# Performance work log

Hardware: AMD Instinct MI355X
Metric: run time of the kernel (lower is better)

The kernel has to match this reference:

```python
import jax, jax.numpy as jnp
import numpy as np

D_MODEL = 2048
NUM_HEADS = 16
HEAD_DIM = D_MODEL // NUM_HEADS
B, S = 2, 2048


def rotate_half(x):
    x1, x2 = jnp.split(x, 2, axis=-1)
    return jnp.concatenate((-x2, x1), axis=-1)


def setup_inputs() -> dict:
    key = jax.random.key(0)
    ks = jax.random.split(key, 7)
    x = jax.random.normal(ks[0], (B, S, D_MODEL), dtype=jnp.float32)
    cos = jax.random.normal(ks[1], (1, 1, S, HEAD_DIM), dtype=jnp.float32)
    sin = jax.random.normal(ks[2], (1, 1, S, HEAD_DIM), dtype=jnp.float32)
    scale = 1.0 / np.sqrt(D_MODEL)
    Wq = jax.random.normal(ks[3], (D_MODEL, D_MODEL), dtype=jnp.float32) * scale
    Wk = jax.random.normal(ks[4], (D_MODEL, D_MODEL), dtype=jnp.float32) * scale
    Wv = jax.random.normal(ks[5], (D_MODEL, D_MODEL), dtype=jnp.float32) * scale
    Wo = jax.random.normal(ks[6], (D_MODEL, D_MODEL), dtype=jnp.float32) * scale
    return {"x": x, "cos": cos, "sin": sin, "Wq": Wq, "Wk": Wk, "Wv": Wv, "Wo": Wo}


def reference(x, cos, sin, Wq, Wk, Wv, Wo):
    Bb, Ss, Dd = x.shape
    H, hd = NUM_HEADS, HEAD_DIM
    # nn.Linear: y = x @ W.T ; here W stored as [out, in]
    q = (x @ Wq.T).reshape(Bb, Ss, H, hd).transpose(0, 2, 1, 3)  # [B,H,S,hd]
    k = (x @ Wk.T).reshape(Bb, Ss, H, hd).transpose(0, 2, 1, 3)
    v = (x @ Wv.T).reshape(Bb, Ss, H, hd).transpose(0, 2, 1, 3)
    q = q * cos + rotate_half(q) * sin
    k = k * cos + rotate_half(k) * sin
    scale = 1.0 / jnp.sqrt(jnp.asarray(hd, dtype=x.dtype))
    scores = jnp.einsum('bhqd,bhkd->bhqk', q, k) * scale  # [B,H,S,S]
    causal = jnp.tril(jnp.ones((Ss, Ss), dtype=bool))
    scores = jnp.where(causal[None, None], scores, jnp.finfo(x.dtype).min)
    attn = jax.nn.softmax(scores, axis=-1)
    out = jnp.einsum('bhqk,bhkd->bhqd', attn, v)  # [B,H,S,hd]
    out = out.transpose(0, 2, 1, 3).reshape(Bb, Ss, Dd)
    return out @ Wo.T
```

## Files before the change

### kernel.cpp

```cpp
#include <hip/hip_runtime.h>

typedef unsigned short u16;
typedef __attribute__((ext_vector_type(8))) short bf8v;
typedef __attribute__((ext_vector_type(4))) float f4v;

#define DEV static __device__ __forceinline__

DEV float bf2f(u16 u){ unsigned x = ((unsigned)u) << 16; float f; __builtin_memcpy(&f, &x, 4); return f; }
DEV u16 f2bf(float f){ unsigned x; __builtin_memcpy(&x, &f, 4); x += 0x7fff + ((x >> 16) & 1); return (u16)(x >> 16); }

DEV void async16(const void* g, void* l){
  __builtin_amdgcn_global_load_lds((const __attribute__((address_space(1))) unsigned*)g,
                                   (__attribute__((address_space(3))) unsigned*)l, 16, 0, 0);
}

DEV void vwait8(){ asm volatile("s_waitcnt vmcnt(8)" ::: "memory"); }
DEV void vwait6(){ asm volatile("s_waitcnt vmcnt(6)" ::: "memory"); }
DEV void vwait0(){ asm volatile("s_waitcnt vmcnt(0)" ::: "memory"); }
DEV void bar(){ asm volatile("s_barrier" ::: "memory"); }

__global__ __launch_bounds__(256) void f2b_k(const float* __restrict__ src,
                                             u16* __restrict__ dst)
{
  const long i = ((long)blockIdx.x * 256 + threadIdx.x) * 4;
  const float4 v = *(const float4*)(src + i);
  ushort4 o;
  o.x = f2bf(v.x); o.y = f2bf(v.y); o.z = f2bf(v.z); o.w = f2bf(v.w);
  *(ushort4*)(dst + i) = o;
}

__global__ __launch_bounds__(256) void f2b3_k(const float* __restrict__ a,
                                              const float* __restrict__ b,
                                              const float* __restrict__ c,
                                              u16* __restrict__ dst)
{
  const int bx = blockIdx.x;
  const float* s = bx < 4096 ? a : (bx < 8192 ? b : c);
  const long soff = ((long)(bx & 4095) * 256 + threadIdx.x) * 4;
  const long doff = ((long)bx * 256 + threadIdx.x) * 4;
  const float4 v = *(const float4*)(s + soff);
  ushort4 o;
  o.x = f2bf(v.x); o.y = f2bf(v.y); o.z = f2bf(v.z); o.w = f2bf(v.w);
  *(ushort4*)(dst + doff) = o;
}

constexpr int KDIM = 2048;

__global__ __launch_bounds__(512, 2) void gemm256(const u16* __restrict__ A,
                                                  const u16* __restrict__ B,
                                                  u16* __restrict__ C0,
                                                  u16* __restrict__ C1,
                                                  u16* __restrict__ C2,
                                                  float* __restrict__ Cf, int mode)
{
  __shared__ __align__(16) u16 Asm[3][8192];
  __shared__ __align__(16) u16 Bsm[3][16384];

  const int tid = threadIdx.x;
  const int w = tid >> 6, lane = tid & 63;
  const int ln = lane & 15, quad = lane >> 4;
  const int wr = w >> 2, wc = w & 3;

  const int gx = gridDim.x;
  const int nwg = gx * gridDim.y;
  const int wg = blockIdx.y * gx + blockIdx.x;
  const int swz = (wg & 7) * (nwg >> 3) + (wg >> 3);
  const int bx = swz % gx, by = swz / gx;
  const long m0 = (long)by << 7, n0 = (long)bx << 8;

  f4v acc[4][4] = {};

  const u16* pA  = A + (m0 + w * 16 + ln) * (long)KDIM + quad * 8;
  const u16* pB0 = B + (n0 + w * 16 + ln) * (long)KDIM + quad * 8;
  const u16* pB1 = B + (n0 + (8 + w) * 16 + ln) * (long)KDIM + quad * 8;
  char* ldsA = (char*)Asm + (long)tid * 16;
  char* ldsB = (char*)Bsm + (long)tid * 16;

#define STG(sl, ks, kt) do{                                                     \
    async16(pA  + (kt) + (ks) * 32, ldsA + (sl) * 16384 + (ks) * 8192);         \
    async16(pB0 + (kt) + (ks) * 32, ldsB + (sl) * 32768 + (ks) * 16384);        \
    async16(pB1 + (kt) + (ks) * 32, ldsB + (sl) * 32768 + (ks) * 16384 + 8192); \
  }while(0)

  STG(0, 0, 0);  STG(0, 1, 0);
  STG(1, 0, 64); STG(1, 1, 64);
  vwait6();
  bar();

  int s0 = 0, s1 = 1, s2 = 2;
  const int nt = KDIM / 64;
  for (int t = 0; t < nt; ++t) {
    const u16* Ab = Asm[s0];
    const u16* Bb = Bsm[s0];
    const bool st = (t + 2 < nt);
    const long kt2 = (long)(t + 2) * 64;

    bf8v a0[4], b0[4];
#pragma unroll
    for (int i = 0; i < 4; ++i) a0[i] = *(const bf8v*)&Ab[((wr * 4 + i) * 64 + lane) * 8];
#pragma unroll
    for (int j = 0; j < 4; ++j) b0[j] = *(const bf8v*)&Bb[((wc * 4 + j) * 64 + lane) * 8];
    if (st) STG(s2, 0, kt2);
    bar();
    __builtin_amdgcn_s_setprio(1);
#pragma unroll
    for (int i = 0; i < 4; ++i)
#pragma unroll
      for (int j = 0; j < 4; ++j)
        acc[i][j] = __builtin_amdgcn_mfma_f32_16x16x32_bf16(a0[i], b0[j], acc[i][j], 0, 0, 0);
    __builtin_amdgcn_s_setprio(0);
    bar();

    bf8v a1[4], b1[4];
#pragma unroll
    for (int i = 0; i < 4; ++i) a1[i] = *(const bf8v*)&Ab[((8 + wr * 4 + i) * 64 + lane) * 8];
#pragma unroll
    for (int j = 0; j < 4; ++j) b1[j] = *(const bf8v*)&Bb[((16 + wc * 4 + j) * 64 + lane) * 8];
    if (st) STG(s2, 1, kt2);
    if (st) vwait6(); else vwait0();
    bar();
    __builtin_amdgcn_s_setprio(1);
#pragma unroll
    for (int i = 0; i < 4; ++i)
#pragma unroll
      for (int j = 0; j < 4; ++j)
        acc[i][j] = __builtin_amdgcn_mfma_f32_16x16x32_bf16(a1[i], b1[j], acc[i][j], 0, 0, 0);
    __builtin_amdgcn_s_setprio(0);
    bar();

    const int tmp = s0; s0 = s1; s1 = s2; s2 = tmp;
  }
#undef STG

#pragma unroll
  for (int i = 0; i < 4; i++) {
    const long mrow = m0 + wr * 64 + i * 16 + quad * 4;
#pragma unroll
    for (int j = 0; j < 4; j++) {
      const long ncol = n0 + wc * 64 + j * 16 + ln;
#pragma unroll
      for (int r = 0; r < 4; r++) {
        const float fv = acc[i][j][r];
        const long m = mrow + r;
        if (mode == 0) {
          C0[m * 2048 + ncol] = f2bf(fv);
        } else if (mode == 2) {
          Cf[m * 2048 + ncol] = fv;
        } else if (mode == 1) {
          const long s = m & 2047, bb = m >> 11;
          const long hh = ncol >> 7, dc = ncol & 127;
          C0[((bb * 16 + hh) * 128 + dc) * 2048 + s] = f2bf(fv);
        } else {
          const int sec = (int)(n0 >> 11);
          const long nc = ncol & 2047;
          if (sec == 0)      C0[m * 2048 + nc] = f2bf(fv);
          else if (sec == 1) C1[m * 2048 + nc] = f2bf(fv);
          else {
            const long s = m & 2047, bb = m >> 11;
            const long hh = nc >> 7, dc = nc & 127;
            C2[((bb * 16 + hh) * 128 + dc) * 2048 + s] = f2bf(fv);
          }
        }
      }
    }
  }
}

__global__ __launch_bounds__(256) void rope2_k(u16* __restrict__ qb,
                                               u16* __restrict__ kb,
                                               const float* __restrict__ cs,
                                               const float* __restrict__ sn)
{
  const long idx = (long)blockIdx.x * 256 + threadIdx.x;
  u16* t = (idx >= 4194304) ? kb : qb;
  const long i2 = idx & 4194303;
  const long m = i2 >> 10;
  const int rest = (int)(i2 & 1023);
  const int h = rest >> 6, d = rest & 63;
  const int s = (int)(m & 2047);
  const long base = m * 2048 + h * 128 + d;
  const float a  = bf2f(t[base]), b = bf2f(t[base + 64]);
  const float c1 = cs[s * 128 + d],      s1 = sn[s * 128 + d];
  const float c2 = cs[s * 128 + d + 64], s2 = sn[s * 128 + d + 64];
  t[base]      = f2bf(a * c1 - b * s1);
  t[base + 64] = f2bf(b * c2 + a * s2);
}

__global__ __launch_bounds__(512) void attn_k(const u16* __restrict__ q,
                                              const u16* __restrict__ k,
                                              const u16* __restrict__ vt,
                                              u16* __restrict__ ao)
{
  __shared__ __align__(16) u16 Ks[2][16384];
  __shared__ __align__(16) u16 Vs[2][16384];
  __shared__ __align__(16) u16 Ps[8 * 16 * 72];
  const int xa = blockIdx.x;
  const int bh = blockIdx.y;
  const int b = bh >> 4, h = bh & 15;
  const int tid = threadIdx.x;
  const int w = tid >> 6, lane = tid & 63;
  const int ln = lane & 15, quad = lane >> 4;

  const u16* kb0 = k + ((long)(b * 2048 + (tid & 15))) * 2048 + h * 128
                     + ((tid >> 6) & 3) * 32 + ((tid >> 4) & 3) * 8;
  const u16* vb0 = vt + ((long)(bh * 128 + (tid & 15))) * 2048
                      + ((tid >> 6) & 1) * 32 + ((tid >> 4) & 3) * 8;
  const int tb = (tid >> 7) & 1;
  const int bit8 = tid >> 8;
  int krow[4]; long voff[4];
#pragma unroll
  for (int it2 = 0; it2 < 4; ++it2) {
    const int ie = 2 * it2 + bit8;
    krow[it2] = (ie >> 2) * 64 + (ie & 3) * 16;
    const int g = 2 * ie + tb;
    voff[it2] = (long)((g & 7) * 16) * 2048 + (g >> 3) * 64;
  }

#define STK(sl, k0) do{                                                          \
    _Pragma("unroll")                                                            \
    for (int it2 = 0; it2 < 4; ++it2)                                            \
      async16(kb0 + (long)((k0) + krow[it2]) * 2048,                             \
              (char*)&Ks[sl][0] + it2 * 8192 + w * 1024);                        \
  }while(0)
#define STV(sl, k0) do{                                                          \
    _Pragma("unroll")                                                            \
    for (int it2 = 0; it2 < 4; ++it2)                                            \
      async16(vb0 + voff[it2] + (k0),                                            \
              (char*)&Vs[sl][0] + it2 * 8192 + w * 1024);                        \
  }while(0)

  const short one_bf = (short)0x3F80;
  const bf8v vones = {one_bf, one_bf, one_bf, one_bf, one_bf, one_bf, one_bf, one_bf};
  const float scl = 0.08838834764831845f;
  const float shift = 20.0f;
  const int wbase = w * 16 * 72;
  const int qts[2] = {15 - xa, xa};

  for (int tix = 0; tix < 2; ++tix) {
    const int qt = qts[tix];
    const int q0 = qt << 7;

    bf8v aq[4];
    {
      const u16* qp = q + ((long)(b * 2048 + q0 + w * 16 + ln)) * 2048 + h * 128;
#pragma unroll
      for (int dt = 0; dt < 4; ++dt) aq[dt] = *(const bf8v*)(qp + dt * 32 + quad * 8);
    }
    f4v O[8] = {};
    f4v Osum = {};

    STK(0, 0); STV(0, 0);

    for (int ktp = 0; ktp <= qt; ++ktp) {
      const int k0s = ktp << 7;
      const bool lastit = (ktp == qt);
      const int sl = ktp & 1;
      if (!lastit) { STK(sl ^ 1, k0s + 128); STV(sl ^ 1, k0s + 128); }
      if (!lastit) vwait8(); else vwait0();
      bar();
      const u16* Kb = &Ks[sl][0];
      const u16* Vb = &Vs[sl][0];

      f4v S[8];
#pragma unroll
      for (int jt = 0; jt < 8; jt++) {
        const int jb = (jt >> 2) * 64 + (jt & 3) * 16;
        if (lastit && jb > w * 16 + 15) {
          S[jt] = (f4v){-1e30f, -1e30f, -1e30f, -1e30f};
          continue;
        }
        const int sub = jt >> 2, jl = jt & 3;
        f4v s = {};
#pragma unroll
        for (int dt = 0; dt < 4; dt++) {
          const bf8v bk = *(const bf8v*)&Kb[(sub * 1024 + (jl * 4 + dt) * 64 + lane) * 8];
          s = __builtin_amdgcn_mfma_f32_16x16x32_bf16(aq[dt], bk, s, 0, 0, 0);
        }
        S[jt] = s;
      }
      if (lastit) {
        const int qi = w * 16 + quad * 4;
#pragma unroll
        for (int jt = 0; jt < 8; jt++) {
          const int dcol = (jt >> 2) * 64 + (jt & 3) * 16 + ln;
#pragma unroll
          for (int r = 0; r < 4; r++) {
            const float arg = (dcol > qi + r) ? -1e30f : (S[jt][r] * scl - shift);
            S[jt][r] = __expf(arg);
          }
        }
      } else {
#pragma unroll
        for (int jt = 0; jt < 8; jt++)
#pragma unroll
          for (int r = 0; r < 4; r++) S[jt][r] = __expf(S[jt][r] * scl - shift);
      }

#pragma unroll
      for (int sub = 0; sub < 2; ++sub) {
        if (sub == 1 && lastit && w < 4) break;
#pragma unroll
        for (int jl = 0; jl < 4; jl++)
#pragma unroll
          for (int r = 0; r < 4; r++)
            Ps[wbase + (quad * 4 + r) * 72 + jl * 16 + ln] = f2bf(S[sub * 4 + jl][r]);
        bf8v ap[2];
#pragma unroll
        for (int k2 = 0; k2 < 2; k2++)
          ap[k2] = *(const bf8v*)&Ps[wbase + ln * 72 + k2 * 32 + quad * 8];
#pragma unroll
        for (int nt = 0; nt < 8; nt++) {
#pragma unroll
          for (int k2 = 0; k2 < 2; k2++) {
            const bf8v bv = *(const bf8v*)&Vb[(sub * 1024 + (nt * 2 + k2) * 64 + lane) * 8];
            O[nt] = __builtin_amdgcn_mfma_f32_16x16x32_bf16(ap[k2], bv, O[nt], 0, 0, 0);
          }
        }
#pragma unroll
        for (int k2 = 0; k2 < 2; k2++)
          Osum = __builtin_amdgcn_mfma_f32_16x16x32_bf16(ap[k2], vones, Osum, 0, 0, 0);
      }
      bar();
    }

    float inv[4];
#pragma unroll
    for (int r = 0; r < 4; r++) inv[r] = 1.0f / Osum[r];
    const long ob = ((long)(b * 2048 + q0 + w * 16 + quad * 4)) * 2048 + h * 128 + ln;
#pragma unroll
    for (int r = 0; r < 4; r++)
#pragma unroll
      for (int nt = 0; nt < 8; nt++)
        ao[ob + (long)r * 2048 + nt * 16] = f2bf(O[nt][r] * inv[r]);
  }
#undef STK
#undef STV
}

extern "C" void kernel_launch(void* const* d_in, const int* in_sizes, int n_in,
                              void* d_out, int out_size, void* d_ws, size_t ws_size,
                              hipStream_t stream) {
  const float* x  = (const float*)d_in[0];
  const float* cs = (const float*)d_in[1];
  const float* sn = (const float*)d_in[2];
  const float* Wq = (const float*)d_in[3];
  const float* Wk = (const float*)d_in[4];
  const float* Wv = (const float*)d_in[5];
  const float* Wo = (const float*)d_in[6];
  float* out = (float*)d_out;

  const size_t E = 4194304;
  u16* xb = (u16*)d_ws;

  const size_t need = 11 * E * sizeof(u16);
  if (ws_size >= need) {
    u16* wqkv = xb + 2 * E;
    u16* qb   = wqkv + 3 * E;
    u16* kb   = qb + 2 * E;
    u16* vtb  = kb + 2 * E;
    u16* aob  = xb;

    f2b_k<<<8192, 256, 0, stream>>>(x, xb);
    f2b3_k<<<12288, 256, 0, stream>>>(Wq, Wk, Wv, wqkv);
    gemm256<<<dim3(24, 32), 512, 0, stream>>>(xb, wqkv, qb, kb, vtb, nullptr, 3);
    rope2_k<<<32768, 256, 0, stream>>>(qb, kb, cs, sn);
    attn_k<<<dim3(8, 32), 512, 0, stream>>>(qb, kb, vtb, aob);
    f2b_k<<<4096, 256, 0, stream>>>(Wo, wqkv);
    gemm256<<<dim3(8, 32), 512, 0, stream>>>(aob, wqkv, nullptr, nullptr, nullptr, out, 2);
  } else {
    u16* wb  = xb + 2 * E;
    u16* qb  = wb + E;
    u16* kb  = qb + 2 * E;
    u16* vtb = kb + 2 * E;
    u16* aob = xb;

    f2b_k<<<8192, 256, 0, stream>>>(x, xb);
    f2b_k<<<4096, 256, 0, stream>>>(Wq, wb);
    gemm256<<<dim3(8, 32), 512, 0, stream>>>(xb, wb, qb, nullptr, nullptr, nullptr, 0);
    f2b_k<<<4096, 256, 0, stream>>>(Wk, wb);
    gemm256<<<dim3(8, 32), 512, 0, stream>>>(xb, wb, kb, nullptr, nullptr, nullptr, 0);
    f2b_k<<<4096, 256, 0, stream>>>(Wv, wb);
    gemm256<<<dim3(8, 32), 512, 0, stream>>>(xb, wb, vtb, nullptr, nullptr, nullptr, 1);
    rope2_k<<<32768, 256, 0, stream>>>(qb, kb, cs, sn);
    attn_k<<<dim3(8, 32), 512, 0, stream>>>(qb, kb, vtb, aob);
    f2b_k<<<4096, 256, 0, stream>>>(Wo, wb);
    gemm256<<<dim3(8, 32), 512, 0, stream>>>(aob, wb, nullptr, nullptr, nullptr, out, 2);
  }
}
```

Before: 478.9 us.

## Add 256x256-tile GEMM with split-phase pipelining for Q/K projection

Adds a new GEMM kernel that computes 256x256 output tiles with a double-buffered LDS pipeline, staging quarter-tiles of A and B interleaved with four MFMA phases. The fused QKV projection is split so that the Q and K columns use this larger-tile kernel and the V columns, with their transposed store, keep the old 128x256 kernel via a new column offset argument. The intent is higher arithmetic intensity and less global/LDS traffic per FLOP for most of the projection. The cost is two launches instead of one, more accumulator registers, and a more intricate wait-count schedule that could stall or add risk.

```diff
diff --git a/kernel.cpp b/kernel.cpp
--- a/kernel.cpp
+++ b/kernel.cpp
@@ -17,6 +17,14 @@
 DEV void vwait8(){ asm volatile("s_waitcnt vmcnt(8)" ::: "memory"); }
 DEV void vwait6(){ asm volatile("s_waitcnt vmcnt(6)" ::: "memory"); }
 DEV void vwait0(){ asm volatile("s_waitcnt vmcnt(0)" ::: "memory"); }
+DEV void vw(int n){
+  switch(n){
+    case 8: asm volatile("s_waitcnt vmcnt(8)" ::: "memory"); break;
+    case 4: asm volatile("s_waitcnt vmcnt(4)" ::: "memory"); break;
+    case 2: asm volatile("s_waitcnt vmcnt(2)" ::: "memory"); break;
+    default: asm volatile("s_waitcnt vmcnt(0)" ::: "memory"); break;
+  }
+}
 DEV void bar(){ asm volatile("s_barrier" ::: "memory"); }
 
 __global__ __launch_bounds__(256) void f2b_k(const float* __restrict__ src,
@@ -46,15 +54,15 @@
 
 constexpr int KDIM = 2048;
 
-__global__ __launch_bounds__(512, 2) void gemm256(const u16* __restrict__ A,
-                                                  const u16* __restrict__ B,
-                                                  u16* __restrict__ C0,
-                                                  u16* __restrict__ C1,
-                                                  u16* __restrict__ C2,
-                                                  float* __restrict__ Cf, int mode)
+__global__ __launch_bounds__(512, 2) void gemmq(const u16* __restrict__ A,
+                                                const u16* __restrict__ B,
+                                                u16* __restrict__ C0,
+                                                u16* __restrict__ C1,
+                                                u16* __restrict__ C2,
+                                                float* __restrict__ Cf, int mode)
 {
-  __shared__ __align__(16) u16 Asm[3][8192];
-  __shared__ __align__(16) u16 Bsm[3][16384];
+  __shared__ __align__(16) u16 Asm[2][16384];
+  __shared__ __align__(16) u16 Bsm[2][16384];
 
   const int tid = threadIdx.x;
   const int w = tid >> 6, lane = tid & 63;
@@ -66,75 +74,128 @@
   const int wg = blockIdx.y * gx + blockIdx.x;
   const int swz = (wg & 7) * (nwg >> 3) + (wg >> 3);
   const int bx = swz % gx, by = swz / gx;
-  const long m0 = (long)by << 7, n0 = (long)bx << 8;
-
-  f4v acc[4][4] = {};
-
-  const u16* pA  = A + (m0 + w * 16 + ln) * (long)KDIM + quad * 8;
-  const u16* pB0 = B + (n0 + w * 16 + ln) * (long)KDIM + quad * 8;
-  const u16* pB1 = B + (n0 + (8 + w) * 16 + ln) * (long)KDIM + quad * 8;
-  char* ldsA = (char*)Asm + (long)tid * 16;
-  char* ldsB = (char*)Bsm + (long)tid * 16;
-
-#define STG(sl, ks, kt) do{                                                     \
-    async16(pA  + (kt) + (ks) * 32, ldsA + (sl) * 16384 + (ks) * 8192);         \
-    async16(pB0 + (kt) + (ks) * 32, ldsB + (sl) * 32768 + (ks) * 16384);        \
-    async16(pB1 + (kt) + (ks) * 32, ldsB + (sl) * 32768 + (ks) * 16384 + 8192); \
-  }while(0)
-
-  STG(0, 0, 0);  STG(0, 1, 0);
-  STG(1, 0, 64); STG(1, 1, 64);
-  vwait6();
+  const long m0 = (long)by << 8, n0 = (long)bx << 8;
+
+  f4v acc[8][4] = {};
+
+  const int q = w >> 1;
+  const int colb = (w & 1) * 32 + quad * 8;
+  long gArow[4], gBrow[4];
+  {
+    const int Ab4[4] = {0, 8, 4, 12};
+    const int Bb4[4] = {0, 8, 2, 10};
+#pragma unroll
+    for (int r = 0; r < 4; ++r) {
+      gArow[r] = (long)((Ab4[r] + q) * 16 + ln) * KDIM;
+      gBrow[r] = (long)((Bb4[r] + (q & 1) + (q >> 1) * 4) * 16 + ln) * KDIM;
+    }
+  }
+  const u16* gA = A + m0 * KDIM + colb;
+  const u16* gB = B + n0 * KDIM + colb;
+
+#define STAGE_A(sl, r, kt) async16(gA + gArow[r] + (kt), (char*)Asm + (sl)*32768 + (r)*8192 + w*1024)
+#define STAGE_B(sl, r, kt) async16(gB + gBrow[r] + (kt), (char*)Bsm + (sl)*32768 + (r)*8192 + w*1024)
+
+  STAGE_A(0,0,0);  STAGE_A(0,1,0);
+  STAGE_B(0,0,0);  STAGE_B(0,1,0);
+  STAGE_B(0,2,0);  STAGE_B(0,3,0);
+  STAGE_A(0,2,0);  STAGE_A(0,3,0);
+  STAGE_A(1,0,64); STAGE_A(1,1,64);
+  STAGE_B(1,0,64); STAGE_B(1,1,64);
+  vwait8();
   bar();
 
-  int s0 = 0, s1 = 1, s2 = 2;
   const int nt = KDIM / 64;
   for (int t = 0; t < nt; ++t) {
-    const u16* Ab = Asm[s0];
-    const u16* Bb = Bsm[s0];
-    const bool st = (t + 2 < nt);
-    const long kt2 = (long)(t + 2) * 64;
-
-    bf8v a0[4], b0[4];
-#pragma unroll
-    for (int i = 0; i < 4; ++i) a0[i] = *(const bf8v*)&Ab[((wr * 4 + i) * 64 + lane) * 8];
-#pragma unroll
-    for (int j = 0; j < 4; ++j) b0[j] = *(const bf8v*)&Bb[((wc * 4 + j) * 64 + lane) * 8];
-    if (st) STG(s2, 0, kt2);
-    bar();
+    const int cs = t & 1;
+    const u16* Ab = Asm[cs];
+    const u16* Bb = Bsm[cs];
+    int w1 = 8, w2 = 8, w3 = 8, w4 = 8;
+    if (t == nt - 2) { w4 = 4; }
+    else if (t == nt - 1) { w1 = 2; w2 = 0; w3 = 0; w4 = 0; }
+    const long kn1 = (long)(t + 1) * 64;
+    const long kn2 = (long)(t + 2) * 64;
+
+    bf8v aL[4][2], aH[4][2], bL[2][2], bH[2][2];
+
+#pragma unroll
+    for (int i = 0; i < 4; ++i) {
+      const int ib = (i + wr * 4) * 2;
+      aL[i][0] = *(const bf8v*)&Ab[((ib + 0) * 64 + lane) * 8];
+      aL[i][1] = *(const bf8v*)&Ab[((ib + 1) * 64 + lane) * 8];
+    }
+#pragma unroll
+    for (int j = 0; j < 2; ++j) {
+      const int jb = (j + wc * 2) * 2;
+      bL[j][0] = *(const bf8v*)&Bb[((jb + 0) * 64 + lane) * 8];
+      bL[j][1] = *(const bf8v*)&Bb[((jb + 1) * 64 + lane) * 8];
+    }
+    if (t + 1 < nt) { STAGE_B(cs ^ 1, 2, kn1); STAGE_B(cs ^ 1, 3, kn1); }
+    vw(w1); bar();
     __builtin_amdgcn_s_setprio(1);
 #pragma unroll
     for (int i = 0; i < 4; ++i)
 #pragma unroll
-      for (int j = 0; j < 4; ++j)
-        acc[i][j] = __builtin_amdgcn_mfma_f32_16x16x32_bf16(a0[i], b0[j], acc[i][j], 0, 0, 0);
+      for (int j = 0; j < 2; ++j) {
+        acc[i][j] = __builtin_amdgcn_mfma_f32_16x16x32_bf16(aL[i][0], bL[j][0], acc[i][j], 0, 0, 0);
+        acc[i][j] = __builtin_amdgcn_mfma_f32_16x16x32_bf16(aL[i][1], bL[j][1], acc[i][j], 0, 0, 0);
+      }
     __builtin_amdgcn_s_setprio(0);
-    bar();
-
-    bf8v a1[4], b1[4];
-#pragma unroll
-    for (int i = 0; i < 4; ++i) a1[i] = *(const bf8v*)&Ab[((8 + wr * 4 + i) * 64 + lane) * 8];
-#pragma unroll
-    for (int j = 0; j < 4; ++j) b1[j] = *(const bf8v*)&Bb[((16 + wc * 4 + j) * 64 + lane) * 8];
-    if (st) STG(s2, 1, kt2);
-    if (st) vwait6(); else vwait0();
-    bar();
+
+#pragma unroll
+    for (int j = 0; j < 2; ++j) {
+      const int jb = ((j & 1) + 8 + wc * 2) * 2;
+      bH[j][0] = *(const bf8v*)&Bb[((jb + 0) * 64 + lane) * 8];
+      bH[j][1] = *(const bf8v*)&Bb[((jb + 1) * 64 + lane) * 8];
+    }
+    if (t + 1 < nt) { STAGE_A(cs ^ 1, 2, kn1); STAGE_A(cs ^ 1, 3, kn1); }
+    vw(w2); bar();
     __builtin_amdgcn_s_setprio(1);
 #pragma unroll
     for (int i = 0; i < 4; ++i)
 #pragma unroll
-      for (int j = 0; j < 4; ++j)
-        acc[i][j] = __builtin_amdgcn_mfma_f32_16x16x32_bf16(a1[i], b1[j], acc[i][j], 0, 0, 0);
+      for (int j = 0; j < 2; ++j) {
+        acc[i][2 + j] = __builtin_amdgcn_mfma_f32_16x16x32_bf16(aL[i][0], bH[j][0], acc[i][2 + j], 0, 0, 0);
+        acc[i][2 + j] = __builtin_amdgcn_mfma_f32_16x16x32_bf16(aL[i][1], bH[j][1], acc[i][2 + j], 0, 0, 0);
+      }
     __builtin_amdgcn_s_setprio(0);
-    bar();
-
-    const int tmp = s0; s0 = s1; s1 = s2; s2 = tmp;
-  }
-#undef STG
-
-#pragma unroll
-  for (int i = 0; i < 4; i++) {
-    const long mrow = m0 + wr * 64 + i * 16 + quad * 4;
+
+#pragma unroll
+    for (int i = 0; i < 4; ++i) {
+      const int ib = (i + 8 + wr * 4) * 2;
+      aH[i][0] = *(const bf8v*)&Ab[((ib + 0) * 64 + lane) * 8];
+      aH[i][1] = *(const bf8v*)&Ab[((ib + 1) * 64 + lane) * 8];
+    }
+    if (t + 2 < nt) { STAGE_A(cs, 0, kn2); STAGE_A(cs, 1, kn2); }
+    vw(w3); bar();
+    __builtin_amdgcn_s_setprio(1);
+#pragma unroll
+    for (int i = 0; i < 4; ++i)
+#pragma unroll
+      for (int j = 0; j < 2; ++j) {
+        acc[4 + i][j] = __builtin_amdgcn_mfma_f32_16x16x32_bf16(aH[i][0], bL[j][0], acc[4 + i][j], 0, 0, 0);
+        acc[4 + i][j] = __builtin_amdgcn_mfma_f32_16x16x32_bf16(aH[i][1], bL[j][1], acc[4 + i][j], 0, 0, 0);
+      }
+    __builtin_amdgcn_s_setprio(0);
+
+    if (t + 2 < nt) { STAGE_B(cs, 0, kn2); STAGE_B(cs, 1, kn2); }
+    vw(w4); bar();
+    __builtin_amdgcn_s_setprio(1);
+#pragma unroll
+    for (int i = 0; i < 4; ++i)
+#pragma unroll
+      for (int j = 0; j < 2; ++j) {
+        acc[4 + i][2 + j] = __builtin_amdgcn_mfma_f32_16x16x32_bf16(aH[i][0], bH[j][0], acc[4 + i][2 + j], 0, 0, 0);
+        acc[4 + i][2 + j] = __builtin_amdgcn_mfma_f32_16x16x32_bf16(aH[i][1], bH[j][1], acc[4 + i][2 + j], 0, 0, 0);
+      }
+    __builtin_amdgcn_s_setprio(0);
+  }
+#undef STAGE_A
+#undef STAGE_B
+
+#pragma unroll
+  for (int i = 0; i < 8; i++) {
+    const long mrow = m0 + wr * 128 + i * 16 + quad * 4;
 #pragma unroll
     for (int j = 0; j < 4; j++) {
       const long ncol = n0 + wc * 64 + j * 16 + ln;
@@ -166,6 +227,127 @@
   }
 }
 
+__global__ __launch_bounds__(512, 2) void gemm256(const u16* __restrict__ A,
+                                                  const u16* __restrict__ B,
+                                                  u16* __restrict__ C0,
+                                                  u16* __restrict__ C1,
+                                                  u16* __restrict__ C2,
+                                                  float* __restrict__ Cf, int mode,
+                                                  int nofs)
+{
+  __shared__ __align__(16) u16 Asm[3][8192];
+  __shared__ __align__(16) u16 Bsm[3][16384];
+
+  const int tid = threadIdx.x;
+  const int w = tid >> 6, lane = tid & 63;
+  const int ln = lane & 15, quad = lane >> 4;
+  const int wr = w >> 2, wc = w & 3;
+
+  const int gx = gridDim.x;
+  const int nwg = gx * gridDim.y;
+  const int wg = blockIdx.y * gx + blockIdx.x;
+  const int swz = (wg & 7) * (nwg >> 3) + (wg >> 3);
+  const int bx = swz % gx, by = swz / gx;
+  const long m0 = (long)by << 7, n0 = ((long)bx << 8) + nofs;
+
+  f4v acc[4][4] = {};
+
+  const u16* pA  = A + (m0 + w * 16 + ln) * (long)KDIM + quad * 8;
+  const u16* pB0 = B + (n0 + w * 16 + ln) * (long)KDIM + quad * 8;
+  const u16* pB1 = B + (n0 + (8 + w) * 16 + ln) * (long)KDIM + quad * 8;
+  char* ldsA = (char*)Asm + (long)tid * 16;
+  char* ldsB = (char*)Bsm + (long)tid * 16;
+
+#define STG(sl, ks, kt) do{                                                     \
+    async16(pA  + (kt) + (ks) * 32, ldsA + (sl) * 16384 + (ks) * 8192);         \
+    async16(pB0 + (kt) + (ks) * 32, ldsB + (sl) * 32768 + (ks) * 16384);        \
+    async16(pB1 + (kt) + (ks) * 32, ldsB + (sl) * 32768 + (ks) * 16384 + 8192); \
+  }while(0)
+
+  STG(0, 0, 0);  STG(0, 1, 0);
+  STG(1, 0, 64); STG(1, 1, 64);
+  vwait6();
+  bar();
+
+  int s0 = 0, s1 = 1, s2 = 2;
+  const int nt = KDIM / 64;
+  for (int t = 0; t < nt; ++t) {
+    const u16* Ab = Asm[s0];
+    const u16* Bb = Bsm[s0];
+    const bool st = (t + 2 < nt);
+    const long kt2 = (long)(t + 2) * 64;
+
+    bf8v a0[4], b0[4];
+#pragma unroll
+    for (int i = 0; i < 4; ++i) a0[i] = *(const bf8v*)&Ab[((wr * 4 + i) * 64 + lane) * 8];
+#pragma unroll
+    for (int j = 0; j < 4; ++j) b0[j] = *(const bf8v*)&Bb[((wc * 4 + j) * 64 + lane) * 8];
+    if (st) STG(s2, 0, kt2);
+    bar();
+    __builtin_amdgcn_s_setprio(1);
+#pragma unroll
+    for (int i = 0; i < 4; ++i)
+#pragma unroll
+      for (int j = 0; j < 4; ++j)
+        acc[i][j] = __builtin_amdgcn_mfma_f32_16x16x32_bf16(a0[i], b0[j], acc[i][j], 0, 0, 0);
+    __builtin_amdgcn_s_setprio(0);
+    bar();
+
+    bf8v a1[4], b1[4];
+#pragma unroll
+    for (int i = 0; i < 4; ++i) a1[i] = *(const bf8v*)&Ab[((8 + wr * 4 + i) * 64 + lane) * 8];
+#pragma unroll
+    for (int j = 0; j < 4; ++j) b1[j] = *(const bf8v*)&Bb[((16 + wc * 4 + j) * 64 + lane) * 8];
+    if (st) STG(s2, 1, kt2);
+    if (st) vwait6(); else vwait0();
+    bar();
+    __builtin_amdgcn_s_setprio(1);
+#pragma unroll
+    for (int i = 0; i < 4; ++i)
+#pragma unroll
+      for (int j = 0; j < 4; ++j)
+        acc[i][j] = __builtin_amdgcn_mfma_f32_16x16x32_bf16(a1[i], b1[j], acc[i][j], 0, 0, 0);
+    __builtin_amdgcn_s_setprio(0);
+    bar();
+
+    const int tmp = s0; s0 = s1; s1 = s2; s2 = tmp;
+  }
+#undef STG
+
+#pragma unroll
+  for (int i = 0; i < 4; i++) {
+    const long mrow = m0 + wr * 64 + i * 16 + quad * 4;
+#pragma unroll
+    for (int j = 0; j < 4; j++) {
+      const long ncol = n0 + wc * 64 + j * 16 + ln;
+#pragma unroll
+      for (int r = 0; r < 4; r++) {
+        const float fv = acc[i][j][r];
+        const long m = mrow + r;
+        if (mode == 0) {
+          C0[m * 2048 + ncol] = f2bf(fv);
+        } else if (mode == 2) {
+          Cf[m * 2048 + ncol] = fv;
+        } else if (mode == 1) {
+          const long s = m & 2047, bb = m >> 11;
+          const long hh = ncol >> 7, dc = ncol & 127;
+          C0[((bb * 16 + hh) * 128 + dc) * 2048 + s] = f2bf(fv);
+        } else {
+          const int sec = (int)(n0 >> 11);
+          const long nc = ncol & 2047;
+          if (sec == 0)      C0[m * 2048 + nc] = f2bf(fv);
+          else if (sec == 1) C1[m * 2048 + nc] = f2bf(fv);
+          else {
+            const long s = m & 2047, bb = m >> 11;
+            const long hh = nc >> 7, dc = nc & 127;
+            C2[((bb * 16 + hh) * 128 + dc) * 2048 + s] = f2bf(fv);
+          }
+        }
+      }
+    }
+  }
+}
+
 __global__ __launch_bounds__(256) void rope2_k(u16* __restrict__ qb,
                                                u16* __restrict__ kb,
                                                const float* __restrict__ cs,
@@ -362,11 +544,12 @@
 
     f2b_k<<<8192, 256, 0, stream>>>(x, xb);
     f2b3_k<<<12288, 256, 0, stream>>>(Wq, Wk, Wv, wqkv);
-    gemm256<<<dim3(24, 32), 512, 0, stream>>>(xb, wqkv, qb, kb, vtb, nullptr, 3);
+    gemmq  <<<dim3(16, 16), 512, 0, stream>>>(xb, wqkv, qb, kb, vtb, nullptr, 3);
+    gemm256<<<dim3(8, 32),  512, 0, stream>>>(xb, wqkv, qb, kb, vtb, nullptr, 3, 4096);
     rope2_k<<<32768, 256, 0, stream>>>(qb, kb, cs, sn);
     attn_k<<<dim3(8, 32), 512, 0, stream>>>(qb, kb, vtb, aob);
     f2b_k<<<4096, 256, 0, stream>>>(Wo, wqkv);
-    gemm256<<<dim3(8, 32), 512, 0, stream>>>(aob, wqkv, nullptr, nullptr, nullptr, out, 2);
+    gemm256<<<dim3(8, 32), 512, 0, stream>>>(aob, wqkv, nullptr, nullptr, nullptr, out, 2, 0);
   } else {
     u16* wb  = xb + 2 * E;
     u16* qb  = wb + E;
@@ -376,14 +559,14 @@
 
     f2b_k<<<8192, 256, 0, stream>>>(x, xb);
     f2b_k<<<4096, 256, 0, stream>>>(Wq, wb);
-    gemm256<<<dim3(8, 32), 512, 0, stream>>>(xb, wb, qb, nullptr, nullptr, nullptr, 0);
+    gemm256<<<dim3(8, 32), 512, 0, stream>>>(xb, wb, qb, nullptr, nullptr, nullptr, 0, 0);
     f2b_k<<<4096, 256, 0, stream>>>(Wk, wb);
-    gemm256<<<dim3(8, 32), 512, 0, stream>>>(xb, wb, kb, nullptr, nullptr, nullptr, 0);
+    gemm256<<<dim3(8, 32), 512, 0, stream>>>(xb, wb, kb, nullptr, nullptr, nullptr, 0, 0);
     f2b_k<<<4096, 256, 0, stream>>>(Wv, wb);
-    gemm256<<<dim3(8, 32), 512, 0, stream>>>(xb, wb, vtb, nullptr, nullptr, nullptr, 1);
+    gemm256<<<dim3(8, 32), 512, 0, stream>>>(xb, wb, vtb, nullptr, nullptr, nullptr, 1, 0);
     rope2_k<<<32768, 256, 0, stream>>>(qb, kb, cs, sn);
     attn_k<<<dim3(8, 32), 512, 0, stream>>>(qb, kb, vtb, aob);
     f2b_k<<<4096, 256, 0, stream>>>(Wo, wb);
-    gemm256<<<dim3(8, 32), 512, 0, stream>>>(aob, wb, nullptr, nullptr, nullptr, out, 2);
-  }
-}
+    gemm256<<<dim3(8, 32), 512, 0, stream>>>(aob, wb, nullptr, nullptr, nullptr, out, 2, 0);
+  }
+}
```

Result: faster. 455.8 us (-4.8%).
